# Kernel optimization log

Hardware: AMD Instinct MI355X
Metric: run time of the kernel (lower is better)

## Reference

```python
import jax, jax.numpy as jnp
import numpy as np

NUM_UNITS = 64
NUM_NODES = 2048
COARSE_NODES = 256
INPUT_DIM = 1
BATCH = 64
AVG_DEGREE = 16


def _normalized_laplacian(adj):
    # A = A + I; L = D^-1/2 A^T D^-1/2 (matches scipy path in source)
    a = adj + np.eye(adj.shape[0], dtype=np.float64)
    d = a.sum(axis=1)
    d_inv_sqrt = np.power(d, -0.5)
    d_inv_sqrt[np.isinf(d_inv_sqrt)] = 0.0
    # (A @ D^-1/2).T @ D^-1/2 = A.T * d[:,None] * d[None,:]
    lap = a.T * d_inv_sqrt[:, None] * d_inv_sqrt[None, :]
    return lap.astype(np.float32)


def _random_adj(rng, n, deg):
    rows = np.repeat(np.arange(n), deg)
    cols = rng.integers(0, n, size=n * deg)
    a = np.zeros((n, n), dtype=np.float64)
    a[rows, cols] = 1.0
    a = np.maximum(a, a.T)  # symmetric
    np.fill_diagonal(a, 0.0)
    return a


def _xavier(key, shape):
    std = np.sqrt(2.0 / (shape[0] + shape[1]))
    return jax.random.normal(key, shape, dtype=jnp.float32) * std


def setup_inputs() -> dict:
    key = jax.random.key(0)
    ks = jax.random.split(key, 8)
    rng = np.random.default_rng(0)

    adj = jnp.asarray(_normalized_laplacian(_random_adj(rng, NUM_NODES, AVG_DEGREE)))
    adj1 = jnp.asarray(_normalized_laplacian(_random_adj(rng, COARSE_NODES, AVG_DEGREE)))
    # afc_mx in source is (num_nodes, coarse_nodes); afc = afc_mx.T, afct = afc_mx
    afc_mx = rng.random((NUM_NODES, COARSE_NODES)).astype(np.float32)
    afc = jnp.asarray(afc_mx.T)   # (C, N)
    afct = jnp.asarray(afc_mx)    # (N, C)

    in_size = INPUT_DIM + NUM_UNITS
    inputs = jax.random.normal(ks[0], (BATCH, NUM_NODES * INPUT_DIM), dtype=jnp.float32)
    state = jax.random.normal(ks[1], (BATCH, NUM_NODES * NUM_UNITS), dtype=jnp.float32)

    return {
        "inputs": inputs, "state": state,
        "adj": adj, "adj1": adj1, "afc": afc, "afct": afct,
        "w0": _xavier(ks[2], (in_size, 2 * NUM_UNITS)),
        "b0": jnp.zeros((2 * NUM_UNITS,), jnp.float32),
        "w1": _xavier(ks[3], (in_size, NUM_UNITS)),
        "b1": jnp.zeros((NUM_UNITS,), jnp.float32),
        "w01": _xavier(ks[4], (in_size, 2 * NUM_UNITS)),
        "b01": jnp.zeros((2 * NUM_UNITS,), jnp.float32),
        "w11": _xavier(ks[5], (in_size, NUM_UNITS)),
        "b11": jnp.zeros((NUM_UNITS,), jnp.float32),
    }


def _gc(inputs, state, adj, adj1, afc, afct, w, b, wf, bf):
    B = inputs.shape[0]
    N, C = adj.shape[0], adj1.shape[0]
    x = jnp.concatenate([inputs.reshape(B, N, -1), state.reshape(B, N, -1)], axis=2)
    F = x.shape[2]
    x0 = x.transpose(1, 2, 0).reshape(N, F * B)          # (N, F*B)
    x0fc = afc @ x0                                      # (C, F*B)
    x1 = adj @ x0                                        # graph conv, fine graph
    x1fc = adj1 @ x0fc                                   # graph conv, coarse graph
    x1 = x1 + jax.nn.sigmoid(afct @ x0fc)                # cross term fine<-coarse
    x1fc = x1fc + jax.nn.sigmoid(afc @ x1)               # cross term coarse<-fine
    out = x1.reshape(N, F, B).transpose(2, 0, 1).reshape(-1, F) @ w + b
    outfc = x1fc.reshape(C, F, B).transpose(2, 0, 1).reshape(-1, F) @ wf + bf
    return out.reshape(B, N, -1), outfc.reshape(B, C, -1)


def reference(inputs, state, adj, adj1, afc, afct, w0, b0, w1, b1, w01, b01, w11, b11):
    B = inputs.shape[0]
    N, U = NUM_NODES, NUM_UNITS
    x1, _x1fc = _gc(inputs, state, adj, adj1, afc, afct, w0, b0, w01, b01)
    value = jax.nn.sigmoid(x1)                           # (B, N, 2U)
    r, u = value[..., :U], value[..., U:]
    r = r.reshape(B, N * U)
    u = u.reshape(B, N * U)
    c0, _c1 = _gc(inputs, r * state, adj, adj1, afc, afct, w1, b1, w11, b11)
    c = jnp.tanh(c0).reshape(B, N * U)
    new_state = u * state + (1.0 - u) * c
    return new_state
```

## Files before the change

### kernel.cpp

```cpp
#include <hip/hip_runtime.h>
#include <hip/hip_bf16.h>
#include <math.h>

#define N_NODES 2048
#define C_NODES 256
#define BATCH   64
#define UNITS   64
#define JS      4096
#define NX      4160
#define JSX     4224
#define NU      131072
#define XSTR    4160
#define CAP     192
#define ZSPLIT  8

typedef short  s16x8 __attribute__((ext_vector_type(8)));
typedef float  f32x4 __attribute__((ext_vector_type(4)));

__device__ __forceinline__ float sigmoidf_(float x) { return 1.0f / (1.0f + __expf(-x)); }

__device__ __forceinline__ float bfs2f(short s) {
    union { float f; unsigned u; } w; w.u = ((unsigned)(unsigned short)s) << 16; return w.f;
}
__device__ __forceinline__ short f2bfs(float f) {
    __hip_bfloat16 h = __float2bfloat16(f);
    short s; __builtin_memcpy(&s, &h, 2); return s;
}

__device__ __forceinline__ void gload_lds16(const void* g, void* l) {
    __builtin_amdgcn_global_load_lds(
        (const __attribute__((address_space(1))) void*)g,
        (__attribute__((address_space(3))) void*)l, 16, 0, 0);
}

__global__ __launch_bounds__(256) void cvt_split(const float* __restrict__ s,
                                                 __hip_bfloat16* __restrict__ dh,
                                                 __hip_bfloat16* __restrict__ dl, int n)
{
    int stride = gridDim.x * 256;
    for (int i = blockIdx.x * 256 + threadIdx.x; i < n; i += stride) {
        float v = s[i];
        __hip_bfloat16 h = __float2bfloat16(v);
        dh[i] = h;
        dl[i] = __float2bfloat16(v - __bfloat162float(h));
    }
}

__global__ __launch_bounds__(256) void cvt_w(const float* __restrict__ w0,
                                             const float* __restrict__ w1,
                                             __hip_bfloat16* __restrict__ w0h, __hip_bfloat16* __restrict__ w0l,
                                             __hip_bfloat16* __restrict__ w1h, __hip_bfloat16* __restrict__ w1l)
{
    int stride = gridDim.x * 256;
    for (int e = blockIdx.x * 256 + threadIdx.x; e < 8192 + 4096; e += stride) {
        if (e < 8192) {
            int jj = e & 7, cell = e >> 3;
            int o = cell & 127, c = cell >> 7;
            float v = w0[(size_t)(1 + c * 8 + jj) * 128 + o];
            __hip_bfloat16 h = __float2bfloat16(v);
            w0h[e] = h; w0l[e] = __float2bfloat16(v - __bfloat162float(h));
        } else {
            int e2 = e - 8192;
            int jj = e2 & 7, cell = e2 >> 3;
            int o = cell & 63, c = cell >> 6;
            float v = w1[(size_t)(1 + c * 8 + jj) * 64 + o];
            __hip_bfloat16 h = __float2bfloat16(v);
            w1h[e2] = h; w1l[e2] = __float2bfloat16(v - __bfloat162float(h));
        }
    }
}

__global__ __launch_bounds__(256) void setup_ext(
    const float* __restrict__ inputs,
    __hip_bfloat16* __restrict__ xh, __hip_bfloat16* __restrict__ xl,
    __hip_bfloat16* __restrict__ fh, __hip_bfloat16* __restrict__ fl,
    __hip_bfloat16* __restrict__ X)
{
    int blk = blockIdx.x;
    if (blk < 64) {
        int b = blk;
        for (int n = threadIdx.x; n < N_NODES; n += 256) {
            float v = inputs[(size_t)b * N_NODES + n];
            __hip_bfloat16 h = __float2bfloat16(v);
            size_t o = (size_t)(JS + b) * N_NODES + n;
            xh[o] = h;
            xl[o] = __float2bfloat16(v - __bfloat162float(h));
            X[(size_t)n * XSTR + 4096 + b] = h;
        }
    } else {
        int r = NX + (blk - 64);
        __hip_bfloat16 z = __float2bfloat16(0.0f);
        for (int n = threadIdx.x; n < N_NODES; n += 256) {
            size_t o = (size_t)r * N_NODES + n;
            xh[o] = z; xl[o] = z;
        }
        for (int c = threadIdx.x; c < C_NODES; c += 256) {
            size_t o = (size_t)r * C_NODES + c;
            fh[o] = z; fl[o] = z;
        }
    }
}

__global__ __launch_bounds__(256) void build_csr(
    const float* __restrict__ adj,
    unsigned short* __restrict__ cols,
    float* __restrict__ vals,
    int* __restrict__ nnz)
{
    int row  = blockIdx.x * 4 + (threadIdx.x >> 6);
    int lane = threadIdx.x & 63;
    const float* a = adj + (size_t)row * N_NODES;
    int base = 0;
    for (int k0 = 0; k0 < N_NODES; k0 += 64) {
        float v = a[k0 + lane];
        unsigned long long m = __ballot(v != 0.0f);
        if (v != 0.0f) {
            int pos = base + __popcll(m & ((1ull << lane) - 1));
            if (pos < CAP) {
                cols[(size_t)row * CAP + pos] = (unsigned short)(k0 + lane);
                vals[(size_t)row * CAP + pos] = v;
            }
        }
        base += __popcll(m);
    }
    if (lane == 0) nnz[row] = base < CAP ? base : CAP;
}

__global__ __launch_bounds__(256) void build_x0sT(const float* __restrict__ st,
                                                  __hip_bfloat16* __restrict__ xh,
                                                  __hip_bfloat16* __restrict__ xl,
                                                  __hip_bfloat16* __restrict__ X)
{
    __shared__ float Ls[64 * 65];
    int n0 = blockIdx.x * 64;
    int b  = blockIdx.y;
    int t  = threadIdx.x;
    #pragma unroll
    for (int it = 0; it < 16; it++) {
        int idx = t + it * 256;
        int i = idx >> 6, u = idx & 63;
        float v = st[(size_t)b * NU + (size_t)(n0 + i) * 64 + u];
        Ls[i * 65 + u] = v;
        X[(size_t)(n0 + i) * XSTR + b * 64 + u] = __float2bfloat16(v);
    }
    __syncthreads();
    #pragma unroll
    for (int it = 0; it < 16; it++) {
        int idx = t + it * 256;
        int u = idx >> 6, i = idx & 63;
        float v = Ls[i * 65 + u];
        __hip_bfloat16 h = __float2bfloat16(v);
        size_t o = (size_t)(b * 64 + u) * N_NODES + n0 + i;
        xh[o] = h;
        xl[o] = __float2bfloat16(v - __bfloat162float(h));
    }
}

__global__ __launch_bounds__(256) void gemm1_mfma128(
    const __hip_bfloat16* __restrict__ Ah, const __hip_bfloat16* __restrict__ Al,
    const __hip_bfloat16* __restrict__ Bh, const __hip_bfloat16* __restrict__ Bl,
    float* __restrict__ part)
{
    __shared__ __align__(16) __hip_bfloat16 S1[8192];
    __shared__ __align__(16) __hip_bfloat16 S2[8192];

    const int K = N_NODES;
    int tid  = threadIdx.x;
    int wave = tid >> 6, lane = tid & 63;
    int quad = lane >> 4, lr = lane & 15;
    int wr = wave >> 1, wc = wave & 1;
    int mBase = blockIdx.y * 128;
    int nBase = blockIdx.x * 128;
    int k0base = blockIdx.z * (K / ZSPLIT);

    int cellkb[4], cellmm[4];
    #pragma unroll
    for (int ch = 0; ch < 4; ch++) {
        int cell = (wave * 4 + ch) * 64 + lane;
        cellkb[ch] = cell >> 7;
        cellmm[ch] = cell & 127;
    }

    f32x4 acc[4][4];
    #pragma unroll
    for (int i = 0; i < 4; i++)
        #pragma unroll
        for (int j = 0; j < 4; j++) { f32x4 z = {0.f,0.f,0.f,0.f}; acc[i][j] = z; }

    const short* Bh_ = (const short*)Bh;
    const short* Bl_ = (const short*)Bl;

    for (int k0 = 0; k0 < K / ZSPLIT; k0 += 64) {
        #pragma unroll
        for (int ch = 0; ch < 4; ch++) {
            size_t offA = (size_t)(mBase + cellmm[ch]) * K + k0base + k0 + cellkb[ch] * 8;
            int lo = (wave * 4 + ch) * 512;
            gload_lds16(Ah + offA, S1 + lo);
            gload_lds16(Al + offA, S2 + lo);
        }
        __syncthreads();
        const s16x8* AhV = (const s16x8*)S1;
        const s16x8* AlV = (const s16x8*)S2;
        #pragma unroll
        for (int ks = 0; ks < 2; ks++) {
            int kb = ks * 4 + quad;
            s16x8 ah[4], al[4];
            #pragma unroll
            for (int i = 0; i < 4; i++) {
                int idx = kb * 128 + wr * 64 + i * 16 + lr;
                ah[i] = AhV[idx]; al[i] = AlV[idx];
            }
            #pragma unroll
            for (int j = 0; j < 4; j++) {
                size_t bo = (size_t)(nBase + wc * 64 + j * 16 + lr) * K + k0base + k0 + kb * 8;
                s16x8 bh = *(const s16x8*)(Bh_ + bo);
                s16x8 bl = *(const s16x8*)(Bl_ + bo);
                #pragma unroll
                for (int i = 0; i < 4; i++) {
                    acc[i][j] = __builtin_amdgcn_mfma_f32_16x16x32_bf16(ah[i], bh, acc[i][j], 0, 0, 0);
                    acc[i][j] = __builtin_amdgcn_mfma_f32_16x16x32_bf16(ah[i], bl, acc[i][j], 0, 0, 0);
                    acc[i][j] = __builtin_amdgcn_mfma_f32_16x16x32_bf16(al[i], bh, acc[i][j], 0, 0, 0);
                }
            }
        }
        __syncthreads();
    }

    float* dst = part + (size_t)blockIdx.z * JSX * C_NODES;
    #pragma unroll
    for (int i = 0; i < 4; i++)
        #pragma unroll
        for (int j = 0; j < 4; j++)
            #pragma unroll
            for (int r = 0; r < 4; r++) {
                int row = mBase + wr * 64 + i * 16 + quad * 4 + r;
                int col = nBase + wc * 64 + j * 16 + lr;
                dst[(size_t)row * C_NODES + col] = acc[i][j][r];
            }
}

__global__ __launch_bounds__(256) void reduce_split(const float* __restrict__ part,
                                                    __hip_bfloat16* __restrict__ oh,
                                                    __hip_bfloat16* __restrict__ ol, int n)
{
    int stride = gridDim.x * 256;
    const size_t slice = (size_t)JSX * C_NODES;
    for (int i = blockIdx.x * 256 + threadIdx.x; i < n; i += stride) {
        float v = 0.f;
        #pragma unroll
        for (int s = 0; s < ZSPLIT; s++) v += part[s * slice + i];
        __hip_bfloat16 h = __float2bfloat16(v);
        oh[i] = h;
        ol[i] = __float2bfloat16(v - __bfloat162float(h));
    }
}

__global__ __launch_bounds__(256, 2) void gemm_coarse(
    const __hip_bfloat16* __restrict__ Ah, const __hip_bfloat16* __restrict__ Al,
    const __hip_bfloat16* __restrict__ Bh, const __hip_bfloat16* __restrict__ Bl,
    __hip_bfloat16* __restrict__ OutH, __hip_bfloat16* __restrict__ OutL)
{
    __shared__ __align__(16) __hip_bfloat16 S1[8192];
    __shared__ __align__(16) __hip_bfloat16 S2[8192];
    __shared__ __align__(16) __hip_bfloat16 S3[8192];
    __shared__ __align__(16) __hip_bfloat16 S4[8192];

    int tid  = threadIdx.x;
    int wave = tid >> 6, lane = tid & 63;
    int quad = lane >> 4, lr = lane & 15;
    int wr = wave >> 1, wc = wave & 1;
    int mBase = blockIdx.y * 128, nBase = blockIdx.x * 128;

    int cellkb[4], cellmm[4];
    #pragma unroll
    for (int ch = 0; ch < 4; ch++) {
        int cell = (wave * 4 + ch) * 64 + lane;
        cellkb[ch] = cell >> 7;
        cellmm[ch] = cell & 127;
    }

    f32x4 acc[4][4];
    #pragma unroll
    for (int i = 0; i < 4; i++)
        #pragma unroll
        for (int j = 0; j < 4; j++) { f32x4 z = {0.f,0.f,0.f,0.f}; acc[i][j] = z; }

    for (int k0 = 0; k0 < C_NODES; k0 += 64) {
        #pragma unroll
        for (int ch = 0; ch < 4; ch++) {
            size_t offA = (size_t)(mBase + cellmm[ch]) * C_NODES + k0 + cellkb[ch] * 8;
            size_t offB = (size_t)(nBase + cellmm[ch]) * C_NODES + k0 + cellkb[ch] * 8;
            int lo = (wave * 4 + ch) * 512;
            gload_lds16(Ah + offA, S1 + lo);
            gload_lds16(Al + offA, S2 + lo);
            gload_lds16(Bh + offB, S3 + lo);
            gload_lds16(Bl + offB, S4 + lo);
        }
        __syncthreads();
        const s16x8* AhV = (const s16x8*)S1;
        const s16x8* AlV = (const s16x8*)S2;
        const s16x8* BhV = (const s16x8*)S3;
        const s16x8* BlV = (const s16x8*)S4;
        #pragma unroll
        for (int ks = 0; ks < 2; ks++) {
            int kb = ks * 4 + quad;
            s16x8 ah[4], al[4], bh[4], bl[4];
            #pragma unroll
            for (int i = 0; i < 4; i++) {
                int idx = kb * 128 + wr * 64 + i * 16 + lr;
                ah[i] = AhV[idx]; al[i] = AlV[idx];
            }
            #pragma unroll
            for (int j = 0; j < 4; j++) {
                int idx = kb * 128 + wc * 64 + j * 16 + lr;
                bh[j] = BhV[idx]; bl[j] = BlV[idx];
            }
            #pragma unroll
            for (int i = 0; i < 4; i++)
                #pragma unroll
                for (int j = 0; j < 4; j++) {
                    acc[i][j] = __builtin_amdgcn_mfma_f32_16x16x32_bf16(ah[i], bh[j], acc[i][j], 0, 0, 0);
                    acc[i][j] = __builtin_amdgcn_mfma_f32_16x16x32_bf16(ah[i], bl[j], acc[i][j], 0, 0, 0);
                    acc[i][j] = __builtin_amdgcn_mfma_f32_16x16x32_bf16(al[i], bh[j], acc[i][j], 0, 0, 0);
                }
        }
        __syncthreads();
    }

    #pragma unroll
    for (int i = 0; i < 4; i++)
        #pragma unroll
        for (int j = 0; j < 4; j++)
            #pragma unroll
            for (int r = 0; r < 4; r++) {
                int row = mBase + wr * 64 + i * 16 + quad * 4 + r;
                int col = nBase + wc * 64 + j * 16 + lr;
                float v = sigmoidf_(acc[i][j][r]);
                size_t idx = (size_t)(col >> 6) * NU + (size_t)row * 64 + (col & 63);
                __hip_bfloat16 h = __float2bfloat16(v);
                OutH[idx] = h;
                OutL[idx] = __float2bfloat16(v - __bfloat162float(h));
            }
}

__global__ __launch_bounds__(256) void spmm_add(
    const __hip_bfloat16* __restrict__ X,
    const unsigned short* __restrict__ cols,
    const float* __restrict__ vals,
    const int* __restrict__ nnz,
    __hip_bfloat16* __restrict__ OutH,
    __hip_bfloat16* __restrict__ OutL)
{
    __shared__ unsigned short colS[4 * CAP];
    __shared__ float          valS[4 * CAP];
    __shared__ int            cntS[4];

    int tid  = threadIdx.x;
    int wave = tid >> 6, lane = tid & 63;
    int wgid = blockIdx.x;
    int jt, nb;
    if (wgid < 4096) { jt = wgid & 7; nb = wgid >> 3; }
    else             { jt = 8;        nb = wgid - 4096; }
    int nBase = nb * 4;

    if (tid < 4) cntS[tid] = nnz[nBase + tid];
    {
        const unsigned short* cpg = cols + (size_t)nBase * CAP;
        const float*          vpg = vals + (size_t)nBase * CAP;
        #pragma unroll
        for (int it = 0; it < 3; it++) {
            int idx = tid + it * 256;
            colS[idx] = cpg[idx];
            valS[idx] = vpg[idx];
        }
    }
    __syncthreads();

    int n   = nBase + wave;
    int cnt = cntS[wave];
    const unsigned short* cp = colS + wave * CAP;
    const float*          vp = valS + wave * CAP;
    const short* Xs = (const short*)X;

    if (jt < 8) {
        int j0 = jt * 512 + lane * 8;
        float acc[8];
        #pragma unroll
        for (int e = 0; e < 8; e++) acc[e] = 0.f;
        int i = 0;
        for (; i + 8 <= cnt; i += 8) {
            int   c[8]; float a[8];
            #pragma unroll
            for (int q = 0; q < 8; q++) { c[q] = cp[i + q]; a[q] = vp[i + q]; }
            s16x8 xv[8];
            #pragma unroll
            for (int q = 0; q < 8; q++)
                xv[q] = *(const s16x8*)(Xs + (size_t)c[q] * XSTR + j0);
            #pragma unroll
            for (int q = 0; q < 8; q++)
                #pragma unroll
                for (int e = 0; e < 8; e++) acc[e] += a[q] * bfs2f(xv[q][e]);
        }
        for (; i < cnt; i++) {
            int c = cp[i]; float a = vp[i];
            s16x8 xv = *(const s16x8*)(Xs + (size_t)c * XSTR + j0);
            #pragma unroll
            for (int e = 0; e < 8; e++) acc[e] += a * bfs2f(xv[e]);
        }
        size_t o = (size_t)(jt * 8 + (lane >> 3)) * NU + (size_t)n * 64 + (lane & 7) * 8;
        s16x8 h = *(const s16x8*)((const short*)OutH + o);
        s16x8 l = *(const s16x8*)((const short*)OutL + o);
        s16x8 nh, nl;
        #pragma unroll
        for (int e = 0; e < 8; e++) {
            float v = bfs2f(h[e]) + bfs2f(l[e]) + acc[e];
            short hh = f2bfs(v);
            nh[e] = hh;
            nl[e] = f2bfs(v - bfs2f(hh));
        }
        *(s16x8*)((short*)OutH + o) = nh;
        *(s16x8*)((short*)OutL + o) = nl;
    } else {
        float acc = 0.f;
        int i = 0;
        for (; i + 8 <= cnt; i += 8) {
            int   c[8]; float a[8];
            #pragma unroll
            for (int q = 0; q < 8; q++) { c[q] = cp[i + q]; a[q] = vp[i + q]; }
            short xv[8];
            #pragma unroll
            for (int q = 0; q < 8; q++) xv[q] = Xs[(size_t)c[q] * XSTR + 4096 + lane];
            #pragma unroll
            for (int q = 0; q < 8; q++) acc += a[q] * bfs2f(xv[q]);
        }
        for (; i < cnt; i++) {
            int c = cp[i]; float a = vp[i];
            acc += a * bfs2f(Xs[(size_t)c * XSTR + 4096 + lane]);
        }
        size_t o = (size_t)64 * NU + (size_t)n * 64 + lane;
        float v = bfs2f(((const short*)OutH)[o]) + bfs2f(((const short*)OutL)[o]) + acc;
        short hh = f2bfs(v);
        ((short*)OutH)[o] = hh;
        ((short*)OutL)[o] = f2bfs(v - bfs2f(hh));
    }
}

__global__ __launch_bounds__(256, 3) void head1_mfma(
    const __hip_bfloat16* __restrict__ x1h, const __hip_bfloat16* __restrict__ x1l,
    const __hip_bfloat16* __restrict__ Wh, const __hip_bfloat16* __restrict__ Wl,
    const float* __restrict__ w0, const float* __restrict__ b0,
    const float* __restrict__ state,
    __hip_bfloat16* __restrict__ xh, __hip_bfloat16* __restrict__ xl,
    __hip_bfloat16* __restrict__ u_buf,
    __hip_bfloat16* __restrict__ Xout)
{
    __shared__ __align__(16) short trH[8192];
    __shared__ __align__(16) short trL[8192];
    __shared__ float xinS[128];

    int n0 = blockIdx.x * 128;
    int b  = blockIdx.y;
    int tid = threadIdx.x;
    int wave = tid >> 6, lane = tid & 63;
    int quad = lane >> 4, lr = lane & 15;
    int wr = wave >> 1, wc = wave & 1;

    if (tid < 128) {
        size_t o = (size_t)64 * NU + (size_t)(n0 + tid) * 64 + b;
        xinS[tid] = __bfloat162float(x1h[o]) + __bfloat162float(x1l[o]);
    }

    f32x4 acc[4][4];
    #pragma unroll
    for (int i = 0; i < 4; i++)
        #pragma unroll
        for (int j = 0; j < 4; j++) { f32x4 z = {0.f,0.f,0.f,0.f}; acc[i][j] = z; }

    const short* Xh = (const short*)x1h + (size_t)b * NU;
    const short* Xl = (const short*)x1l + (size_t)b * NU;
    const short* Wh_ = (const short*)Wh;
    const short* Wl_ = (const short*)Wl;

    #pragma unroll
    for (int ks = 0; ks < 2; ks++) {
        s16x8 ah[4], al[4];
        #pragma unroll
        for (int i = 0; i < 4; i++) {
            size_t off = (size_t)(n0 + wr * 64 + i * 16 + lr) * 64 + ks * 32 + quad * 8;
            ah[i] = *(const s16x8*)(Xh + off);
            al[i] = *(const s16x8*)(Xl + off);
        }
        #pragma unroll
        for (int j = 0; j < 4; j++) {
            size_t wo = ((size_t)(ks * 4 + quad) * 128 + wc * 64 + j * 16 + lr) * 8;
            s16x8 bh = *(const s16x8*)(Wh_ + wo);
            s16x8 bl = *(const s16x8*)(Wl_ + wo);
            #pragma unroll
            for (int i = 0; i < 4; i++) {
                acc[i][j] = __builtin_amdgcn_mfma_f32_16x16x32_bf16(ah[i], bh, acc[i][j], 0, 0, 0);
                acc[i][j] = __builtin_amdgcn_mfma_f32_16x16x32_bf16(ah[i], bl, acc[i][j], 0, 0, 0);
                acc[i][j] = __builtin_amdgcn_mfma_f32_16x16x32_bf16(al[i], bh, acc[i][j], 0, 0, 0);
            }
        }
    }
    __syncthreads();

    if (wc == 0) {
        #pragma unroll
        for (int i = 0; i < 4; i++) {
            float sv[4][4];
            #pragma unroll
            for (int j = 0; j < 4; j++)
                #pragma unroll
                for (int r = 0; r < 4; r++)
                    sv[j][r] = state[(size_t)b * NU
                                     + (size_t)(n0 + wr * 64 + i * 16 + quad * 4 + r) * 64
                                     + j * 16 + lr];
            #pragma unroll
            for (int j = 0; j < 4; j++)
                #pragma unroll
                for (int r = 0; r < 4; r++) {
                    int n_loc = wr * 64 + i * 16 + quad * 4 + r;
                    int o = j * 16 + lr;
                    float g = acc[i][j][r] + w0[o] * xinS[n_loc] + b0[o];
                    float sg = sigmoidf_(g);
                    float rs = sg * sv[j][r];
                    short h = f2bfs(rs);
                    int sw = n_loc ^ ((o & 15) << 3);
                    trH[o * 128 + sw] = h;
                    trL[o * 128 + sw] = f2bfs(rs - bfs2f(h));
                    ((short*)Xout)[(size_t)(n0 + n_loc) * XSTR + b * 64 + o] = h;
                }
        }
    } else {
        #pragma unroll
        for (int i = 0; i < 4; i++)
            #pragma unroll
            for (int j = 0; j < 4; j++)
                #pragma unroll
                for (int r = 0; r < 4; r++) {
                    int n_loc = wr * 64 + i * 16 + quad * 4 + r;
                    int o = 64 + j * 16 + lr;
                    float g = acc[i][j][r] + w0[o] * xinS[n_loc] + b0[o];
                    float sg = sigmoidf_(g);
                    u_buf[(size_t)b * NU + (size_t)(n0 + n_loc) * 64 + (o - 64)] = __float2bfloat16(sg);
                }
    }
    __syncthreads();

    {
        int row = tid >> 2, seg = tid & 3;
        int xorv = (row & 15) << 3;
        short* dh = (short*)xh + (size_t)(b * 64 + row) * N_NODES + n0 + seg * 32;
        short* dl = (short*)xl + (size_t)(b * 64 + row) * N_NODES + n0 + seg * 32;
        #pragma unroll
        for (int q = 0; q < 4; q++) {
            int src = row * 128 + ((seg * 32 + q * 8) ^ xorv);
            *(uint4*)(dh + q * 8) = *(const uint4*)(trH + src);
            *(uint4*)(dl + q * 8) = *(const uint4*)(trL + src);
        }
    }
}

__global__ __launch_bounds__(256, 3) void head2_mfma(
    const __hip_bfloat16* __restrict__ x1h, const __hip_bfloat16* __restrict__ x1l,
    const __hip_bfloat16* __restrict__ Wh, const __hip_bfloat16* __restrict__ Wl,
    const float* __restrict__ w1, const float* __restrict__ b1,
    const float* __restrict__ state, const __hip_bfloat16* __restrict__ u_buf,
    float* __restrict__ out)
{
    __shared__ float xinS[128];

    int n0 = blockIdx.x * 128;
    int b  = blockIdx.y;
    int tid = threadIdx.x;
    int wave = tid >> 6, lane = tid & 63;
    int quad = lane >> 4, lr = lane & 15;

    if (tid < 128) {
        size_t o = (size_t)64 * NU + (size_t)(n0 + tid) * 64 + b;
        xinS[tid] = __bfloat162float(x1h[o]) + __bfloat162float(x1l[o]);
    }

    f32x4 acc[2][4];
    #pragma unroll
    for (int i = 0; i < 2; i++)
        #pragma unroll
        for (int j = 0; j < 4; j++) { f32x4 z = {0.f,0.f,0.f,0.f}; acc[i][j] = z; }

    const short* Xh = (const short*)x1h + (size_t)b * NU;
    const short* Xl = (const short*)x1l + (size_t)b * NU;
    const short* Wh_ = (const short*)Wh;
    const short* Wl_ = (const short*)Wl;

    #pragma unroll
    for (int ks = 0; ks < 2; ks++) {
        s16x8 ah[2], al[2];
        #pragma unroll
        for (int i = 0; i < 2; i++) {
            size_t off = (size_t)(n0 + wave * 32 + i * 16 + lr) * 64 + ks * 32 + quad * 8;
            ah[i] = *(const s16x8*)(Xh + off);
            al[i] = *(const s16x8*)(Xl + off);
        }
        #pragma unroll
        for (int j = 0; j < 4; j++) {
            size_t wo = ((size_t)(ks * 4 + quad) * 64 + j * 16 + lr) * 8;
            s16x8 bh = *(const s16x8*)(Wh_ + wo);
            s16x8 bl = *(const s16x8*)(Wl_ + wo);
            #pragma unroll
            for (int i = 0; i < 2; i++) {
                acc[i][j] = __builtin_amdgcn_mfma_f32_16x16x32_bf16(ah[i], bh, acc[i][j], 0, 0, 0);
                acc[i][j] = __builtin_amdgcn_mfma_f32_16x16x32_bf16(ah[i], bl, acc[i][j], 0, 0, 0);
                acc[i][j] = __builtin_amdgcn_mfma_f32_16x16x32_bf16(al[i], bh, acc[i][j], 0, 0, 0);
            }
        }
    }
    __syncthreads();

    float sv[2][4][4];
    float uv[2][4][4];
    #pragma unroll
    for (int i = 0; i < 2; i++)
        #pragma unroll
        for (int j = 0; j < 4; j++)
            #pragma unroll
            for (int r = 0; r < 4; r++) {
                size_t sidx = (size_t)b * NU
                            + (size_t)(n0 + wave * 32 + i * 16 + quad * 4 + r) * 64
                            + j * 16 + lr;
                sv[i][j][r] = state[sidx];
                uv[i][j][r] = __bfloat162float(u_buf[sidx]);
            }

    #pragma unroll
    for (int i = 0; i < 2; i++)
        #pragma unroll
        for (int j = 0; j < 4; j++)
            #pragma unroll
            for (int r = 0; r < 4; r++) {
                int n_loc = wave * 32 + i * 16 + quad * 4 + r;
                int o = j * 16 + lr;
                float g = acc[i][j][r] + w1[o] * xinS[n_loc] + b1[o];
                float c = tanhf(g);
                size_t sidx = (size_t)b * NU + (size_t)(n0 + n_loc) * 64 + o;
                float ug = uv[i][j][r];
                float svv = sv[i][j][r];
                out[sidx] = ug * svv + (1.0f - ug) * c;
            }
}

extern "C" void kernel_launch(void* const* d_in, const int* in_sizes, int n_in,
                              void* d_out, int out_size, void* d_ws, size_t ws_size,
                              hipStream_t stream)
{
    const float* inputs = (const float*)d_in[0];
    const float* state  = (const float*)d_in[1];
    const float* adj    = (const float*)d_in[2];
    const float* afc    = (const float*)d_in[4];
    const float* afct   = (const float*)d_in[5];
    const float* w0     = (const float*)d_in[6];
    const float* b0     = (const float*)d_in[7];
    const float* w1     = (const float*)d_in[8];
    const float* b1     = (const float*)d_in[9];

    float* out = (float*)d_out;

    char* p = (char*)d_ws;
    __hip_bfloat16* afc_h    = (__hip_bfloat16*)p; p += (size_t)C_NODES * N_NODES * 2;
    __hip_bfloat16* afc_l    = (__hip_bfloat16*)p; p += (size_t)C_NODES * N_NODES * 2;
    __hip_bfloat16* afct_h   = (__hip_bfloat16*)p; p += (size_t)N_NODES * C_NODES * 2;
    __hip_bfloat16* afct_l   = (__hip_bfloat16*)p; p += (size_t)N_NODES * C_NODES * 2;
    __hip_bfloat16* w0T_h    = (__hip_bfloat16*)p; p += 8192 * 2;
    __hip_bfloat16* w0T_l    = (__hip_bfloat16*)p; p += 8192 * 2;
    __hip_bfloat16* w1T_h    = (__hip_bfloat16*)p; p += 4096 * 2;
    __hip_bfloat16* w1T_l    = (__hip_bfloat16*)p; p += 4096 * 2;
    __hip_bfloat16* x0sT_h   = (__hip_bfloat16*)p; p += (size_t)JSX * N_NODES * 2;
    __hip_bfloat16* x0sT_l   = (__hip_bfloat16*)p; p += (size_t)JSX * N_NODES * 2;
    __hip_bfloat16* x0fcT_h  = (__hip_bfloat16*)p; p += (size_t)JSX * C_NODES * 2;
    __hip_bfloat16* x0fcT_l  = (__hip_bfloat16*)p; p += (size_t)JSX * C_NODES * 2;
    float*          part     = (float*)p;
    __hip_bfloat16* x1B_h    = (__hip_bfloat16*)p; p += (size_t)66 * NU * 2;
    __hip_bfloat16* x1B_l    = (__hip_bfloat16*)p; p += (size_t)66 * NU * 2;
    __hip_bfloat16* u_buf    = (__hip_bfloat16*)p; p += (size_t)BATCH * NU * 2;
    __hip_bfloat16* X        = (__hip_bfloat16*)p; p += (size_t)N_NODES * XSTR * 2;
    unsigned short* csr_cols = (unsigned short*)p; p += (size_t)N_NODES * CAP * 2;
    float*          csr_vals = (float*)p;          p += (size_t)N_NODES * CAP * 4;
    int*            csr_nnz  = (int*)p;            p += (size_t)N_NODES * 4;

    dim3 blk(256);

    cvt_split<<<256,  blk, 0, stream>>>(afc,  afc_h,  afc_l,  C_NODES * N_NODES);
    cvt_split<<<256,  blk, 0, stream>>>(afct, afct_h, afct_l, N_NODES * C_NODES);
    cvt_w    <<<32,   blk, 0, stream>>>(w0, w1, w0T_h, w0T_l, w1T_h, w1T_l);
    setup_ext<<<128,  blk, 0, stream>>>(inputs, x0sT_h, x0sT_l, x0fcT_h, x0fcT_l, X);
    build_csr<<<512,  blk, 0, stream>>>(adj, csr_cols, csr_vals, csr_nnz);

    build_x0sT<<<dim3(32, 64), blk, 0, stream>>>(state, x0sT_h, x0sT_l, X);
    gemm1_mfma128<<<dim3(2, 33, ZSPLIT), blk, 0, stream>>>(x0sT_h, x0sT_l, afc_h, afc_l, part);
    reduce_split<<<1024, blk, 0, stream>>>(part, x0fcT_h, x0fcT_l, NX * C_NODES);
    gemm_coarse<<<dim3(33, 16), blk, 0, stream>>>(afct_h, afct_l, x0fcT_h, x0fcT_l, x1B_h, x1B_l);
    spmm_add<<<dim3(4608), blk, 0, stream>>>(X, csr_cols, csr_vals, csr_nnz, x1B_h, x1B_l);
    head1_mfma<<<dim3(16, 64), blk, 0, stream>>>(x1B_h, x1B_l, w0T_h, w0T_l, w0, b0,
                                                 state, x0sT_h, x0sT_l, u_buf, X);

    gemm1_mfma128<<<dim3(2, 33, ZSPLIT), blk, 0, stream>>>(x0sT_h, x0sT_l, afc_h, afc_l, part);
    reduce_split<<<1024, blk, 0, stream>>>(part, x0fcT_h, x0fcT_l, NX * C_NODES);
    gemm_coarse<<<dim3(33, 16), blk, 0, stream>>>(afct_h, afct_l, x0fcT_h, x0fcT_l, x1B_h, x1B_l);
    spmm_add<<<dim3(4608), blk, 0, stream>>>(X, csr_cols, csr_vals, csr_nnz, x1B_h, x1B_l);
    head2_mfma<<<dim3(16, 64), blk, 0, stream>>>(x1B_h, x1B_l, w1T_h, w1T_l, w1, b1,
                                                 state, u_buf, out);
}
```

Measured before the change: 462.8 us.

## Double-buffer A tiles in LDS and prefetch B fragments in gemm1

Splits the A-operand LDS staging in gemm1_mfma128 into two buffers. The next k-tile's global-to-LDS loads are issued before the MFMAs on the current tile, so load latency overlaps with compute. All B fragments for a k-tile are also loaded into registers up front instead of inside the inner loop. The cost is double the LDS (64KB per block) and more live registers, which may reduce occupancy.

```diff
diff --git a/kernel.cpp b/kernel.cpp
--- a/kernel.cpp
+++ b/kernel.cpp
@@ -161,8 +161,8 @@
     const __hip_bfloat16* __restrict__ Bh, const __hip_bfloat16* __restrict__ Bl,
     float* __restrict__ part)
 {
-    __shared__ __align__(16) __hip_bfloat16 S1[8192];
-    __shared__ __align__(16) __hip_bfloat16 S2[8192];
+    __shared__ __align__(16) __hip_bfloat16 S1[2][8192];
+    __shared__ __align__(16) __hip_bfloat16 S2[2][8192];
 
     const int K = N_NODES;
     int tid  = threadIdx.x;
@@ -173,12 +173,13 @@
     int nBase = blockIdx.x * 128;
     int k0base = blockIdx.z * (K / ZSPLIT);
 
-    int cellkb[4], cellmm[4];
+    size_t offA[4]; int lo[4];
     #pragma unroll
     for (int ch = 0; ch < 4; ch++) {
         int cell = (wave * 4 + ch) * 64 + lane;
-        cellkb[ch] = cell >> 7;
-        cellmm[ch] = cell & 127;
+        int kb = cell >> 7, mm = cell & 127;
+        offA[ch] = (size_t)(mBase + mm) * K + k0base + kb * 8;
+        lo[ch] = (wave * 4 + ch) * 512;
     }
 
     f32x4 acc[4][4];
@@ -190,17 +191,39 @@
     const short* Bh_ = (const short*)Bh;
     const short* Bl_ = (const short*)Bl;
 
-    for (int k0 = 0; k0 < K / ZSPLIT; k0 += 64) {
-        #pragma unroll
-        for (int ch = 0; ch < 4; ch++) {
-            size_t offA = (size_t)(mBase + cellmm[ch]) * K + k0base + k0 + cellkb[ch] * 8;
-            int lo = (wave * 4 + ch) * 512;
-            gload_lds16(Ah + offA, S1 + lo);
-            gload_lds16(Al + offA, S2 + lo);
-        }
-        __syncthreads();
-        const s16x8* AhV = (const s16x8*)S1;
-        const s16x8* AlV = (const s16x8*)S2;
+    #pragma unroll
+    for (int ch = 0; ch < 4; ch++) {
+        gload_lds16(Ah + offA[ch], &S1[0][lo[ch]]);
+        gload_lds16(Al + offA[ch], &S2[0][lo[ch]]);
+    }
+    __syncthreads();
+
+    #pragma unroll 1
+    for (int t = 0; t < 4; t++) {
+        int cur = t & 1;
+
+        s16x8 bh[2][4], bl[2][4];
+        #pragma unroll
+        for (int ks = 0; ks < 2; ks++) {
+            int kb = ks * 4 + quad;
+            #pragma unroll
+            for (int j = 0; j < 4; j++) {
+                size_t bo = (size_t)(nBase + wc * 64 + j * 16 + lr) * K + k0base + t * 64 + kb * 8;
+                bh[ks][j] = *(const s16x8*)(Bh_ + bo);
+                bl[ks][j] = *(const s16x8*)(Bl_ + bo);
+            }
+        }
+
+        if (t < 3) {
+            #pragma unroll
+            for (int ch = 0; ch < 4; ch++) {
+                gload_lds16(Ah + offA[ch] + (t + 1) * 64, &S1[cur ^ 1][lo[ch]]);
+                gload_lds16(Al + offA[ch] + (t + 1) * 64, &S2[cur ^ 1][lo[ch]]);
+            }
+        }
+
+        const s16x8* AhV = (const s16x8*)S1[cur];
+        const s16x8* AlV = (const s16x8*)S2[cur];
         #pragma unroll
         for (int ks = 0; ks < 2; ks++) {
             int kb = ks * 4 + quad;
@@ -211,17 +234,13 @@
                 ah[i] = AhV[idx]; al[i] = AlV[idx];
             }
             #pragma unroll
-            for (int j = 0; j < 4; j++) {
-                size_t bo = (size_t)(nBase + wc * 64 + j * 16 + lr) * K + k0base + k0 + kb * 8;
-                s16x8 bh = *(const s16x8*)(Bh_ + bo);
-                s16x8 bl = *(const s16x8*)(Bl_ + bo);
+            for (int j = 0; j < 4; j++)
                 #pragma unroll
                 for (int i = 0; i < 4; i++) {
-                    acc[i][j] = __builtin_amdgcn_mfma_f32_16x16x32_bf16(ah[i], bh, acc[i][j], 0, 0, 0);
-                    acc[i][j] = __builtin_amdgcn_mfma_f32_16x16x32_bf16(ah[i], bl, acc[i][j], 0, 0, 0);
-                    acc[i][j] = __builtin_amdgcn_mfma_f32_16x16x32_bf16(al[i], bh, acc[i][j], 0, 0, 0);
+                    acc[i][j] = __builtin_amdgcn_mfma_f32_16x16x32_bf16(ah[i], bh[ks][j], acc[i][j], 0, 0, 0);
+                    acc[i][j] = __builtin_amdgcn_mfma_f32_16x16x32_bf16(ah[i], bl[ks][j], acc[i][j], 0, 0, 0);
+                    acc[i][j] = __builtin_amdgcn_mfma_f32_16x16x32_bf16(al[i], bh[ks][j], acc[i][j], 0, 0, 0);
                 }
-            }
         }
         __syncthreads();
     }
```

Result: no change. 458.5 us (median of 2 runs) (-0.9%).

## Replace LDS-staged split-K GEMM with register-direct loads and reordered block mapping

Applied to the files above, without the earlier changes.

The first coarse-projection GEMM no longer stages the A operand through shared memory with barriers. Each wave now loads both A and B fragments straight from global memory into registers and runs the full 256-wide K slice fully unrolled. The grid is flattened to 1D so that consecutive workgroups share the same column block and walk through the K splits together, which is meant to improve L2 reuse. This drops LDS traffic and synchronisation, but each wave re-reads A from global memory instead of sharing it across the block, and register pressure rises.

```diff
diff --git a/kernel.cpp b/kernel.cpp
--- a/kernel.cpp
+++ b/kernel.cpp
@@ -156,77 +156,70 @@
     }
 }
 
-__global__ __launch_bounds__(256) void gemm1_mfma128(
+__global__ __launch_bounds__(256) void gemm1_reg(
     const __hip_bfloat16* __restrict__ Ah, const __hip_bfloat16* __restrict__ Al,
     const __hip_bfloat16* __restrict__ Bh, const __hip_bfloat16* __restrict__ Bl,
     float* __restrict__ part)
 {
-    __shared__ __align__(16) __hip_bfloat16 S1[8192];
-    __shared__ __align__(16) __hip_bfloat16 S2[8192];
-
     const int K = N_NODES;
     int tid  = threadIdx.x;
     int wave = tid >> 6, lane = tid & 63;
     int quad = lane >> 4, lr = lane & 15;
     int wr = wave >> 1, wc = wave & 1;
-    int mBase = blockIdx.y * 128;
-    int nBase = blockIdx.x * 128;
-    int k0base = blockIdx.z * (K / ZSPLIT);
-
-    int cellkb[4], cellmm[4];
-    #pragma unroll
-    for (int ch = 0; ch < 4; ch++) {
-        int cell = (wave * 4 + ch) * 64 + lane;
-        cellkb[ch] = cell >> 7;
-        cellmm[ch] = cell & 127;
-    }
-
-    f32x4 acc[4][4];
-    #pragma unroll
-    for (int i = 0; i < 4; i++)
-        #pragma unroll
-        for (int j = 0; j < 4; j++) { f32x4 z = {0.f,0.f,0.f,0.f}; acc[i][j] = z; }
-
+
+    int wgid = blockIdx.x;
+    int cblk = wgid / 264;
+    int rest = wgid % 264;
+    int mblk = rest >> 3;
+    int zblk = rest & 7;
+    int mBase = mblk * 128;
+    int nBase = cblk * 128;
+    int k0base = zblk * (K / ZSPLIT);
+
+    const short* Ah_ = (const short*)Ah;
+    const short* Al_ = (const short*)Al;
     const short* Bh_ = (const short*)Bh;
     const short* Bl_ = (const short*)Bl;
 
-    for (int k0 = 0; k0 < K / ZSPLIT; k0 += 64) {
-        #pragma unroll
-        for (int ch = 0; ch < 4; ch++) {
-            size_t offA = (size_t)(mBase + cellmm[ch]) * K + k0base + k0 + cellkb[ch] * 8;
-            int lo = (wave * 4 + ch) * 512;
-            gload_lds16(Ah + offA, S1 + lo);
-            gload_lds16(Al + offA, S2 + lo);
-        }
-        __syncthreads();
-        const s16x8* AhV = (const s16x8*)S1;
-        const s16x8* AlV = (const s16x8*)S2;
-        #pragma unroll
-        for (int ks = 0; ks < 2; ks++) {
-            int kb = ks * 4 + quad;
-            s16x8 ah[4], al[4];
-            #pragma unroll
-            for (int i = 0; i < 4; i++) {
-                int idx = kb * 128 + wr * 64 + i * 16 + lr;
-                ah[i] = AhV[idx]; al[i] = AlV[idx];
-            }
+    size_t aoff[4], boff[4];
+    #pragma unroll
+    for (int i = 0; i < 4; i++)
+        aoff[i] = (size_t)(mBase + wr * 64 + i * 16 + lr) * K + k0base + quad * 8;
+    #pragma unroll
+    for (int j = 0; j < 4; j++)
+        boff[j] = (size_t)(nBase + wc * 64 + j * 16 + lr) * K + k0base + quad * 8;
+
+    f32x4 acc[4][4];
+    #pragma unroll
+    for (int i = 0; i < 4; i++)
+        #pragma unroll
+        for (int j = 0; j < 4; j++) { f32x4 z = {0.f,0.f,0.f,0.f}; acc[i][j] = z; }
+
+    #pragma unroll
+    for (int ks = 0; ks < 8; ks++) {
+        int ko = ks * 32;
+        s16x8 ah[4], al[4], bh[4], bl[4];
+        #pragma unroll
+        for (int i = 0; i < 4; i++) {
+            ah[i] = *(const s16x8*)(Ah_ + aoff[i] + ko);
+            al[i] = *(const s16x8*)(Al_ + aoff[i] + ko);
+        }
+        #pragma unroll
+        for (int j = 0; j < 4; j++) {
+            bh[j] = *(const s16x8*)(Bh_ + boff[j] + ko);
+            bl[j] = *(const s16x8*)(Bl_ + boff[j] + ko);
+        }
+        #pragma unroll
+        for (int i = 0; i < 4; i++)
             #pragma unroll
             for (int j = 0; j < 4; j++) {
-                size_t bo = (size_t)(nBase + wc * 64 + j * 16 + lr) * K + k0base + k0 + kb * 8;
-                s16x8 bh = *(const s16x8*)(Bh_ + bo);
-                s16x8 bl = *(const s16x8*)(Bl_ + bo);
-                #pragma unroll
-                for (int i = 0; i < 4; i++) {
-                    acc[i][j] = __builtin_amdgcn_mfma_f32_16x16x32_bf16(ah[i], bh, acc[i][j], 0, 0, 0);
-                    acc[i][j] = __builtin_amdgcn_mfma_f32_16x16x32_bf16(ah[i], bl, acc[i][j], 0, 0, 0);
-                    acc[i][j] = __builtin_amdgcn_mfma_f32_16x16x32_bf16(al[i], bh, acc[i][j], 0, 0, 0);
-                }
-            }
-        }
-        __syncthreads();
-    }
-
-    float* dst = part + (size_t)blockIdx.z * JSX * C_NODES;
+                acc[i][j] = __builtin_amdgcn_mfma_f32_16x16x32_bf16(ah[i], bh[j], acc[i][j], 0, 0, 0);
+                acc[i][j] = __builtin_amdgcn_mfma_f32_16x16x32_bf16(ah[i], bl[j], acc[i][j], 0, 0, 0);
+                acc[i][j] = __builtin_amdgcn_mfma_f32_16x16x32_bf16(al[i], bh[j], acc[i][j], 0, 0, 0);
+            }
+    }
+
+    float* dst = part + (size_t)zblk * JSX * C_NODES;
     #pragma unroll
     for (int i = 0; i < 4; i++)
         #pragma unroll
@@ -696,14 +689,14 @@
     build_csr<<<512,  blk, 0, stream>>>(adj, csr_cols, csr_vals, csr_nnz);
 
     build_x0sT<<<dim3(32, 64), blk, 0, stream>>>(state, x0sT_h, x0sT_l, X);
-    gemm1_mfma128<<<dim3(2, 33, ZSPLIT), blk, 0, stream>>>(x0sT_h, x0sT_l, afc_h, afc_l, part);
+    gemm1_reg<<<dim3(528), blk, 0, stream>>>(x0sT_h, x0sT_l, afc_h, afc_l, part);
     reduce_split<<<1024, blk, 0, stream>>>(part, x0fcT_h, x0fcT_l, NX * C_NODES);
     gemm_coarse<<<dim3(33, 16), blk, 0, stream>>>(afct_h, afct_l, x0fcT_h, x0fcT_l, x1B_h, x1B_l);
     spmm_add<<<dim3(4608), blk, 0, stream>>>(X, csr_cols, csr_vals, csr_nnz, x1B_h, x1B_l);
     head1_mfma<<<dim3(16, 64), blk, 0, stream>>>(x1B_h, x1B_l, w0T_h, w0T_l, w0, b0,
                                                  state, x0sT_h, x0sT_l, u_buf, X);
 
-    gemm1_mfma128<<<dim3(2, 33, ZSPLIT), blk, 0, stream>>>(x0sT_h, x0sT_l, afc_h, afc_l, part);
+    gemm1_reg<<<dim3(528), blk, 0, stream>>>(x0sT_h, x0sT_l, afc_h, afc_l, part);
     reduce_split<<<1024, blk, 0, stream>>>(part, x0fcT_h, x0fcT_l, NX * C_NODES);
     gemm_coarse<<<dim3(33, 16), blk, 0, stream>>>(afct_h, afct_l, x0fcT_h, x0fcT_l, x1B_h, x1B_l);
     spmm_add<<<dim3(4608), blk, 0, stream>>>(X, csr_cols, csr_vals, csr_nnz, x1B_h, x1B_l);
```

After: 472.3 us. 1.02x slower.
